# Performance work log

Measured on AMD Instinct MI355X. Metric: run time of the kernel, lower is better.

Reference implementation:

```python
import jax, jax.numpy as jnp
import numpy as np

D_MODEL = 512
NUM_HEADS = 8
WINDOW = 64
HEAD_DIM = D_MODEL // NUM_HEADS


def setup_inputs() -> dict:
    key = jax.random.key(0)
    k1, k2, k3 = jax.random.split(key, 3)
    B, F, L, D = 4, 16, 2048, D_MODEL
    x = jax.random.normal(k1, (B, F, L, D), dtype=jnp.float32)
    w_qkv = jax.random.normal(k2, (D, 3 * D), dtype=jnp.float32) * (1.0 / np.sqrt(D))
    b_qkv = jnp.zeros((3 * D,), dtype=jnp.float32)
    w_proj = jax.random.normal(k3, (D, D), dtype=jnp.float32) * (1.0 / np.sqrt(D))
    b_proj = jnp.zeros((D,), dtype=jnp.float32)
    return {"x": x, "w_qkv": w_qkv, "b_qkv": b_qkv, "w_proj": w_proj, "b_proj": b_proj}


def reference(x, w_qkv, b_qkv, w_proj, b_proj):
    B, F, L, D = x.shape
    W = WINDOW
    H, hd = NUM_HEADS, HEAD_DIM
    nw = L // W  # L chosen divisible by window_size; pad path is identity here
    # partition into windows: (B, F, nw, W, D)
    xw = x.reshape(B, F, nw, W, D)
    # fused QKV projection
    qkv = jnp.einsum('bfnwd,de->bfnwe', xw, w_qkv) + b_qkv  # (B,F,nw,W,3D)
    qkv = qkv.reshape(B, F, nw, W, 3, H, hd)
    q = qkv[..., 0, :, :]  # (B,F,nw,W,H,hd)
    k = qkv[..., 1, :, :]
    v = qkv[..., 2, :, :]
    scale = 1.0 / np.sqrt(hd).astype(np.float32)
    # per-window attention: scores (B,F,nw,H,W,W)
    scores = jnp.einsum('bfnqhd,bfnkhd->bfnhqk', q, k) * scale
    attn = jax.nn.softmax(scores, axis=-1)
    out = jnp.einsum('bfnhqk,bfnkhd->bfnqhd', attn, v)  # (B,F,nw,W,H,hd)
    out = out.reshape(B, F, nw, W, D)
    out = jnp.einsum('bfnwd,de->bfnwe', out, w_proj) + b_proj
    return out.reshape(B, F, L, D)
```

## Files before the change

### kernel.cpp

```cpp
#include <hip/hip_runtime.h>

typedef __attribute__((ext_vector_type(8))) short short8;
typedef __attribute__((ext_vector_type(4))) float f32x4;
typedef unsigned short u16;
typedef unsigned int u32;

__device__ __forceinline__ u16 f2bf(float f){
  union { float f; u32 u; } v; v.f = f;
  u32 u = v.u;
  u32 r = (u + 0x7FFFu + ((u >> 16) & 1u)) >> 16;
  return (u16)r;
}

__device__ __forceinline__ int swz(int row, int cb){ return cb ^ ((row & 7) << 4); }

__device__ __forceinline__ void gload16(const void* g, void* l){
  __builtin_amdgcn_global_load_lds(
      (const __attribute__((address_space(1))) unsigned int*)g,
      (__attribute__((address_space(3))) unsigned int*)l, 16, 0, 0);
}

__global__ void convert_weights_swz(const float* __restrict__ wqkv,
                                    const float* __restrict__ wproj,
                                    u16* __restrict__ wq_swz,
                                    u16* __restrict__ wpt){
  int c = blockIdx.x * 256 + threadIdx.x;
  union { u16 u[8]; uint4 v; } t;
  if (c < 98304){
    int tile = c >> 10, row = (c >> 3) & 127, c7 = c & 7;
    int bn = tile >> 3, kt = tile & 7;
    int j  = c7 ^ (row & 7);
    int e  = bn * 128 + row;
    int k0 = kt * 64 + j * 8;
    #pragma unroll
    for (int i = 0; i < 8; ++i) t.u[i] = f2bf(wqkv[(long)(k0 + i) * 1536 + e]);
    *reinterpret_cast<uint4*>(wq_swz + (long)c * 8) = t.v;
  } else {
    int t2 = c - 98304;
    int cc = t2 >> 6;
    int kc = (t2 & 63) << 3;
    #pragma unroll
    for (int i = 0; i < 8; ++i) t.u[i] = f2bf(wproj[(long)(kc + i) * 512 + cc]);
    *reinterpret_cast<uint4*>(wpt + (long)cc * 512 + kc) = t.v;
  }
}

__global__ void convert_x(const float* __restrict__ x, u16* __restrict__ xbf){
  int c = blockIdx.x * 256 + threadIdx.x;
  int tile = c >> 10, row = (c >> 3) & 127, c7 = c & 7;
  int bm = tile >> 3, kt = tile & 7;
  int j  = c7 ^ (row & 7);
  const float* src = x + (long)(bm * 128 + row) * 512 + kt * 64 + j * 8;
  float4 v0 = *reinterpret_cast<const float4*>(src);
  float4 v1 = *reinterpret_cast<const float4*>(src + 4);
  union { u16 u[8]; uint4 v; } t;
  t.u[0] = f2bf(v0.x); t.u[1] = f2bf(v0.y); t.u[2] = f2bf(v0.z); t.u[3] = f2bf(v0.w);
  t.u[4] = f2bf(v1.x); t.u[5] = f2bf(v1.y); t.u[6] = f2bf(v1.z); t.u[7] = f2bf(v1.w);
  *reinterpret_cast<uint4*>(xbf + (long)c * 8) = t.v;
}

__global__ __launch_bounds__(256) void qkv_gemm(
    const u16*  __restrict__ xbf,
    const u16*  __restrict__ wswz,
    const float* __restrict__ bqkv,
    u16* __restrict__ qkv)
{
  __shared__ char smem[34816];
  char* ldsA = smem;
  char* ldsB = smem + 16384;
  u16*  ldsC = (u16*)smem;

  int hb   = blockIdx.x;
  int work = (hb & 7) * 1536 + (hb >> 3);
  int bn   = work % 12;
  int bm   = work / 12;

  const int tid = threadIdx.x;
  const int l = tid & 63, w = tid >> 6;
  const int g = l >> 4,  ln = l & 15;
  const int wm = w >> 1, wn = w & 1;

  f32x4 acc[4][4];
  #pragma unroll
  for (int m = 0; m < 4; ++m)
    #pragma unroll
    for (int n = 0; n < 4; ++n) acc[m][n] = (f32x4){0.f,0.f,0.f,0.f};

  const char* abase = (const char*)(xbf  + (long)(bm * 8) * 8192);
  const char* bbase = (const char*)(wswz + (long)(bn * 8) * 8192);

  for (int kt = 0; kt < 8; ++kt){
    __syncthreads();
    #pragma unroll
    for (int i = 0; i < 4; ++i){
      gload16(abase + (long)kt*16384 + (i*256 + tid)*16, ldsA + (i*256 + w*64)*16);
      gload16(bbase + (long)kt*16384 + (i*256 + tid)*16, ldsB + (i*256 + w*64)*16);
    }
    __syncthreads();
    #pragma unroll
    for (int ks = 0; ks < 2; ++ks){
      short8 a[4], b[4];
      #pragma unroll
      for (int m = 0; m < 4; ++m){
        int row = wm*64 + m*16 + ln;
        a[m] = *reinterpret_cast<const short8*>(ldsA + row*128 + (((ks*4 + g) ^ (row & 7)) << 4));
      }
      #pragma unroll
      for (int n = 0; n < 4; ++n){
        int row = wn*64 + n*16 + ln;
        b[n] = *reinterpret_cast<const short8*>(ldsB + row*128 + (((ks*4 + g) ^ (row & 7)) << 4));
      }
      #pragma unroll
      for (int m = 0; m < 4; ++m)
        #pragma unroll
        for (int n = 0; n < 4; ++n)
          acc[m][n] = __builtin_amdgcn_mfma_f32_16x16x32_bf16(a[m], b[n], acc[m][n], 0, 0, 0);
    }
  }

  __syncthreads();
  #pragma unroll
  for (int n = 0; n < 4; ++n){
    int col  = wn*64 + n*16 + ln;
    float bias = bqkv[bn*128 + col];
    #pragma unroll
    for (int m = 0; m < 4; ++m){
      int r0 = wm*64 + m*16 + g*4;
      #pragma unroll
      for (int r = 0; r < 4; ++r)
        ldsC[(r0 + r) * 136 + col] = f2bf(acc[m][n][r] + bias);
    }
  }
  __syncthreads();
  {
    int row = tid >> 1, half = tid & 1;
    const char* src = (const char*)(ldsC + row * 136 + half * 64);
    char* dst = (char*)qkv + ((long)(bm*128 + row) * 1536 + bn*128 + half*64) * 2;
    #pragma unroll
    for (int j = 0; j < 8; ++j)
      *reinterpret_cast<uint4*>(dst + j*16) = *reinterpret_cast<const uint4*>(src + j*16);
  }
}

__global__ __launch_bounds__(512, 2) void winattn_proj(
    const u16* __restrict__ qkv,
    const u16* __restrict__ wpt,
    const float* __restrict__ bproj,
    float* __restrict__ out)
{
  __shared__ u16 lds[8][2][4096];
  const int tid = threadIdx.x;
  const int l = tid & 63, w = tid >> 6;
  const int g = l >> 4,  ln = l & 15;
  const long tokb = (long)blockIdx.x * 64;
  u16* vt = lds[w][0];
  u16* pp = lds[w][1];
  const int h = w;

  short8 qa[4][2], kb[4][2];
  #pragma unroll
  for (int m = 0; m < 4; ++m){
    const char* qrow = (const char*)(qkv + (tokb + m*16 + ln) * 1536 + h*64 + g*8);
    const char* krow = (const char*)(qkv + (tokb + m*16 + ln) * 1536 + 512 + h*64 + g*8);
    qa[m][0] = *reinterpret_cast<const short8*>(qrow);
    qa[m][1] = *reinterpret_cast<const short8*>(qrow + 64);
    kb[m][0] = *reinterpret_cast<const short8*>(krow);
    kb[m][1] = *reinterpret_cast<const short8*>(krow + 64);
  }
  const int dg = l & 3, tg = l >> 2;
  uint4 vr[4][2];
  #pragma unroll
  for (int r = 0; r < 4; ++r){
    const char* vrow = (const char*)(qkv + (tokb + tg*4 + r) * 1536 + 1024 + h*64 + dg*16);
    vr[r][0] = *reinterpret_cast<const uint4*>(vrow);
    vr[r][1] = *reinterpret_cast<const uint4*>(vrow + 16);
  }
  f32x4 sacc[4][4];
  #pragma unroll
  for (int m = 0; m < 4; ++m)
    #pragma unroll
    for (int n = 0; n < 4; ++n) sacc[m][n] = (f32x4){0.f,0.f,0.f,0.f};
  #pragma unroll
  for (int ks = 0; ks < 2; ++ks)
    #pragma unroll
    for (int m = 0; m < 4; ++m)
      #pragma unroll
      for (int n = 0; n < 4; ++n)
        sacc[m][n] = __builtin_amdgcn_mfma_f32_16x16x32_bf16(qa[m][ks], kb[n][ks], sacc[m][n], 0, 0, 0);
  #pragma unroll
  for (int dd = 0; dd < 16; ++dd){
    int d = dg*16 + dd;
    int sub = dd & 7, hh = dd >> 3;
    uint2 pk;
    pk.x = (u32)((const u16*)&vr[0][hh])[sub] | ((u32)((const u16*)&vr[1][hh])[sub] << 16);
    pk.y = (u32)((const u16*)&vr[2][hh])[sub] | ((u32)((const u16*)&vr[3][hh])[sub] << 16);
    *reinterpret_cast<uint2*>((char*)vt + d*128 + swz(d, tg*8)) = pk;
  }
  #pragma unroll
  for (int m = 0; m < 4; ++m){
    #pragma unroll
    for (int r = 0; r < 4; ++r){
      float mx = fmaxf(fmaxf(sacc[m][0][r], sacc[m][1][r]), fmaxf(sacc[m][2][r], sacc[m][3][r]));
      mx = fmaxf(mx, __shfl_xor(mx, 1, 64));
      mx = fmaxf(mx, __shfl_xor(mx, 2, 64));
      mx = fmaxf(mx, __shfl_xor(mx, 4, 64));
      mx = fmaxf(mx, __shfl_xor(mx, 8, 64));
      float p[4], s = 0.f;
      #pragma unroll
      for (int n = 0; n < 4; ++n){
        p[n] = __expf((sacc[m][n][r] - mx) * 0.125f);
        s += p[n];
      }
      s += __shfl_xor(s, 1, 64);
      s += __shfl_xor(s, 2, 64);
      s += __shfl_xor(s, 4, 64);
      s += __shfl_xor(s, 8, 64);
      float inv = 1.f / s;
      int i = m*16 + g*4 + r;
      #pragma unroll
      for (int n = 0; n < 4; ++n){
        int c = n*16 + ln;
        *reinterpret_cast<u16*>((char*)pp + i*128 + swz(i, c*2)) = f2bf(p[n] * inv);
      }
    }
  }
  f32x4 oacc[4][4];
  #pragma unroll
  for (int m = 0; m < 4; ++m)
    #pragma unroll
    for (int n = 0; n < 4; ++n) oacc[m][n] = (f32x4){0.f,0.f,0.f,0.f};
  #pragma unroll
  for (int ks = 0; ks < 2; ++ks){
    short8 pa[4], vb[4];
    #pragma unroll
    for (int m = 0; m < 4; ++m){
      int row = m*16 + ln;
      pa[m] = *reinterpret_cast<const short8*>((char*)pp + row*128 + swz(row, (ks*32 + g*8)*2));
    }
    #pragma unroll
    for (int n = 0; n < 4; ++n){
      int row = n*16 + ln;
      vb[n] = *reinterpret_cast<const short8*>((char*)vt + row*128 + swz(row, (ks*32 + g*8)*2));
    }
    #pragma unroll
    for (int m = 0; m < 4; ++m)
      #pragma unroll
      for (int n = 0; n < 4; ++n)
        oacc[m][n] = __builtin_amdgcn_mfma_f32_16x16x32_bf16(pa[m], vb[n], oacc[m][n], 0, 0, 0);
  }
  #pragma unroll
  for (int m = 0; m < 4; ++m)
    #pragma unroll
    for (int n = 0; n < 4; ++n){
      int d = n*16 + ln;
      #pragma unroll
      for (int r = 0; r < 4; ++r){
        int t = m*16 + g*4 + r;
        *reinterpret_cast<u16*>((char*)pp + t*128 + swz(t, d*2)) = f2bf(oacc[m][n][r]);
      }
    }

  __syncthreads();

  f32x4 acc[4][4];
  #pragma unroll
  for (int m = 0; m < 4; ++m)
    #pragma unroll
    for (int n = 0; n < 4; ++n) acc[m][n] = (f32x4){0.f,0.f,0.f,0.f};

  for (int hh = 0; hh < 8; ++hh){
    const char* obuf = (const char*)lds[hh][1];
    #pragma unroll
    for (int ks = 0; ks < 2; ++ks){
      short8 a[4], b[4];
      #pragma unroll
      for (int m = 0; m < 4; ++m){
        int row = m*16 + ln;
        a[m] = *reinterpret_cast<const short8*>(obuf + row*128 + swz(row, (ks*32 + g*8)*2));
      }
      #pragma unroll
      for (int n = 0; n < 4; ++n){
        int e = w*64 + n*16 + ln;
        b[n] = *reinterpret_cast<const short8*>(wpt + (long)e*512 + hh*64 + ks*32 + g*8);
      }
      #pragma unroll
      for (int m = 0; m < 4; ++m)
        #pragma unroll
        for (int n = 0; n < 4; ++n)
          acc[m][n] = __builtin_amdgcn_mfma_f32_16x16x32_bf16(a[m], b[n], acc[m][n], 0, 0, 0);
    }
  }

  #pragma unroll
  for (int n = 0; n < 4; ++n){
    int col = w*64 + n*16 + ln;
    float bias = bproj[col];
    #pragma unroll
    for (int m = 0; m < 4; ++m){
      #pragma unroll
      for (int r = 0; r < 4; ++r){
        int t = m*16 + g*4 + r;
        out[(tokb + t) * 512 + col] = acc[m][n][r] + bias;
      }
    }
  }
}

__global__ void convert_weights(const float* __restrict__ wqkv,
                                const float* __restrict__ wproj,
                                u16* __restrict__ wqkvt,
                                u16* __restrict__ wprojt){
  int tid = blockIdx.x * 256 + threadIdx.x;
  union { u16 u[8]; uint4 v; } tmp;
  if (tid < 1536 * 64){
    int e  = tid >> 6;
    int kc = (tid & 63) << 3;
    #pragma unroll
    for (int i = 0; i < 8; ++i) tmp.u[i] = f2bf(wqkv[(long)(kc + i) * 1536 + e]);
    *reinterpret_cast<uint4*>(wqkvt + (long)e * 512 + kc) = tmp.v;
  } else {
    int t2 = tid - 1536 * 64;
    int c  = t2 >> 6;
    int kc = (t2 & 63) << 3;
    #pragma unroll
    for (int i = 0; i < 8; ++i) tmp.u[i] = f2bf(wproj[(long)(kc + i) * 512 + c]);
    *reinterpret_cast<uint4*>(wprojt + (long)c * 512 + kc) = tmp.v;
  }
}

__global__ __launch_bounds__(512, 2) void fused_winattn(
    const float* __restrict__ x,
    const u16*  __restrict__ wqkvt,
    const float* __restrict__ bqkv,
    const u16*  __restrict__ wprojt,
    const float* __restrict__ bproj,
    float* __restrict__ out)
{
  __shared__ u16 lds_x[64 * 512];
  __shared__ u16 lds_q[64 * 64];
  __shared__ u16 lds_k[64 * 64];
  __shared__ u16 lds_vt[64 * 64];
  __shared__ u16 lds_p[64 * 64];

  const int tid = threadIdx.x;
  const int l   = tid & 63;
  const int w   = tid >> 6;
  const int g   = l >> 4;
  const int ln  = l & 15;
  const long tokbase = (long)blockIdx.x * 64;

  {
    const float4* xv = reinterpret_cast<const float4*>(x + tokbase * 512);
    #pragma unroll
    for (int j = 0; j < 16; ++j){
      int i   = j * 512 + tid;
      int row = i >> 7;
      int c4  = i & 127;
      float4 v = xv[i];
      uint2 pk;
      pk.x = (u32)f2bf(v.x) | ((u32)f2bf(v.y) << 16);
      pk.y = (u32)f2bf(v.z) | ((u32)f2bf(v.w) << 16);
      int byte = row * 1024 + swz(row, c4 * 8);
      *reinterpret_cast<uint2*>(reinterpret_cast<char*>(lds_x) + byte) = pk;
    }
  }

  f32x4 oacc[4][4];
  #pragma unroll
  for (int m = 0; m < 4; ++m)
    #pragma unroll
    for (int n = 0; n < 4; ++n) oacc[m][n] = (f32x4){0.f, 0.f, 0.f, 0.f};

  const int mw   = w & 3;
  const int half = w >> 2;

  __syncthreads();

  for (int h = 0; h < 8; ++h){
    f32x4 qacc[6];
    #pragma unroll
    for (int j = 0; j < 6; ++j) qacc[j] = (f32x4){0.f, 0.f, 0.f, 0.f};
    int ebase[6];
    #pragma unroll
    for (int j = 0; j < 6; ++j){
      int nt = half * 6 + j;
      int sec = nt >> 2;
      ebase[j] = sec * 512 + h * 64 + (nt & 3) * 16;
    }
    const int arow = mw * 16 + ln;
    #pragma unroll
    for (int ks = 0; ks < 16; ++ks){
      short8 a = *reinterpret_cast<const short8*>(
          reinterpret_cast<const char*>(lds_x) + arow * 1024 + swz(arow, (ks * 32 + g * 8) * 2));
      #pragma unroll
      for (int j = 0; j < 6; ++j){
        short8 b = *reinterpret_cast<const short8*>(
            wqkvt + (long)(ebase[j] + ln) * 512 + ks * 32 + g * 8);
        qacc[j] = __builtin_amdgcn_mfma_f32_16x16x32_bf16(a, b, qacc[j], 0, 0, 0);
      }
    }
    #pragma unroll
    for (int j = 0; j < 6; ++j){
      int nt  = half * 6 + j;
      int sec = nt >> 2;
      float bias = bqkv[ebase[j] + ln];
      if (sec < 2){
        u16* dst = (sec == 0) ? lds_q : lds_k;
        int c = (nt & 3) * 16 + ln;
        #pragma unroll
        for (int r = 0; r < 4; ++r){
          int t = mw * 16 + g * 4 + r;
          int byte = t * 128 + swz(t, c * 2);
          *reinterpret_cast<u16*>(reinterpret_cast<char*>(dst) + byte) = f2bf(qacc[j][r] + bias);
        }
      } else {
        int d  = (nt & 3) * 16 + ln;
        int t0 = mw * 16 + g * 4;
        uint2 pk;
        pk.x = (u32)f2bf(qacc[j][0] + bias) | ((u32)f2bf(qacc[j][1] + bias) << 16);
        pk.y = (u32)f2bf(qacc[j][2] + bias) | ((u32)f2bf(qacc[j][3] + bias) << 16);
        int byte = d * 128 + swz(d, t0 * 2);
        *reinterpret_cast<uint2*>(reinterpret_cast<char*>(lds_vt) + byte) = pk;
      }
    }
    __syncthreads();

    if (w < 4){
      f32x4 sacc[4];
      #pragma unroll
      for (int jt = 0; jt < 4; ++jt) sacc[jt] = (f32x4){0.f, 0.f, 0.f, 0.f};
      #pragma unroll
      for (int ks = 0; ks < 2; ++ks){
        int qrow = w * 16 + ln;
        short8 a = *reinterpret_cast<const short8*>(
            reinterpret_cast<const char*>(lds_q) + qrow * 128 + swz(qrow, (ks * 32 + g * 8) * 2));
        #pragma unroll
        for (int jt = 0; jt < 4; ++jt){
          int krow = jt * 16 + ln;
          short8 b = *reinterpret_cast<const short8*>(
              reinterpret_cast<const char*>(lds_k) + krow * 128 + swz(krow, (ks * 32 + g * 8) * 2));
          sacc[jt] = __builtin_amdgcn_mfma_f32_16x16x32_bf16(a, b, sacc[jt], 0, 0, 0);
        }
      }
      #pragma unroll
      for (int r = 0; r < 4; ++r){
        float mx = fmaxf(fmaxf(sacc[0][r], sacc[1][r]), fmaxf(sacc[2][r], sacc[3][r]));
        mx = fmaxf(mx, __shfl_xor(mx, 1, 64));
        mx = fmaxf(mx, __shfl_xor(mx, 2, 64));
        mx = fmaxf(mx, __shfl_xor(mx, 4, 64));
        mx = fmaxf(mx, __shfl_xor(mx, 8, 64));
        float p[4], s = 0.f;
        #pragma unroll
        for (int jt = 0; jt < 4; ++jt){
          p[jt] = __expf((sacc[jt][r] - mx) * 0.125f);
          s += p[jt];
        }
        s += __shfl_xor(s, 1, 64);
        s += __shfl_xor(s, 2, 64);
        s += __shfl_xor(s, 4, 64);
        s += __shfl_xor(s, 8, 64);
        float inv = 1.f / s;
        int i = w * 16 + g * 4 + r;
        #pragma unroll
        for (int jt = 0; jt < 4; ++jt){
          int c = jt * 16 + ln;
          int byte = i * 128 + swz(i, c * 2);
          *reinterpret_cast<u16*>(reinterpret_cast<char*>(lds_p) + byte) = f2bf(p[jt] * inv);
        }
      }
    }
    __syncthreads();

    {
      int mc  = w & 3;
      int nc0 = (w >> 2) * 2;
      f32x4 oc[2];
      oc[0] = (f32x4){0.f, 0.f, 0.f, 0.f};
      oc[1] = (f32x4){0.f, 0.f, 0.f, 0.f};
      #pragma unroll
      for (int ks = 0; ks < 2; ++ks){
        int prow = mc * 16 + ln;
        short8 a = *reinterpret_cast<const short8*>(
            reinterpret_cast<const char*>(lds_p) + prow * 128 + swz(prow, (ks * 32 + g * 8) * 2));
        #pragma unroll
        for (int jj = 0; jj < 2; ++jj){
          int vrow = (nc0 + jj) * 16 + ln;
          short8 b = *reinterpret_cast<const short8*>(
              reinterpret_cast<const char*>(lds_vt) + vrow * 128 + swz(vrow, (ks * 32 + g * 8) * 2));
          oc[jj] = __builtin_amdgcn_mfma_f32_16x16x32_bf16(a, b, oc[jj], 0, 0, 0);
        }
      }
      #pragma unroll
      for (int jj = 0; jj < 2; ++jj){
        int d = (nc0 + jj) * 16 + ln;
        #pragma unroll
        for (int r = 0; r < 4; ++r){
          int t = mc * 16 + g * 4 + r;
          int byte = t * 128 + swz(t, d * 2);
          *reinterpret_cast<u16*>(reinterpret_cast<char*>(lds_q) + byte) = f2bf(oc[jj][r]);
        }
      }
    }
    __syncthreads();

    #pragma unroll
    for (int ks = 0; ks < 2; ++ks){
      short8 a[4];
      #pragma unroll
      for (int m = 0; m < 4; ++m){
        int row = m * 16 + ln;
        a[m] = *reinterpret_cast<const short8*>(
            reinterpret_cast<const char*>(lds_q) + row * 128 + swz(row, (ks * 32 + g * 8) * 2));
      }
      #pragma unroll
      for (int nt = 0; nt < 4; ++nt){
        int e = w * 64 + nt * 16 + ln;
        short8 b = *reinterpret_cast<const short8*>(
            wprojt + (long)e * 512 + h * 64 + ks * 32 + g * 8);
        #pragma unroll
        for (int m = 0; m < 4; ++m)
          oacc[m][nt] = __builtin_amdgcn_mfma_f32_16x16x32_bf16(a[m], b, oacc[m][nt], 0, 0, 0);
      }
    }
    __syncthreads();
  }

  #pragma unroll
  for (int nt = 0; nt < 4; ++nt){
    int col = w * 64 + nt * 16 + ln;
    float bias = bproj[col];
    #pragma unroll
    for (int m = 0; m < 4; ++m){
      #pragma unroll
      for (int r = 0; r < 4; ++r){
        int t = m * 16 + g * 4 + r;
        out[(tokbase + t) * 512 + col] = oacc[m][nt][r] + bias;
      }
    }
  }
}

extern "C" void kernel_launch(void* const* d_in, const int* in_sizes, int n_in,
                              void* d_out, int out_size, void* d_ws, size_t ws_size,
                              hipStream_t stream) {
  const float* x     = (const float*)d_in[0];
  const float* wqkv  = (const float*)d_in[1];
  const float* bqkv  = (const float*)d_in[2];
  const float* wproj = (const float*)d_in[3];
  const float* bproj = (const float*)d_in[4];
  float* out = (float*)d_out;

  const size_t NEED = 538968064ULL;
  if (ws_size >= NEED){
    u16* wq_swz = (u16*)d_ws;
    u16* wpt    = (u16*)((char*)d_ws + 1572864);
    u16* xbf    = (u16*)((char*)d_ws + 2097152);
    u16* qkv    = (u16*)((char*)d_ws + 136314880);
    convert_weights_swz<<<512, 256, 0, stream>>>(wqkv, wproj, wq_swz, wpt);
    convert_x<<<32768, 256, 0, stream>>>(x, xbf);
    qkv_gemm<<<12288, 256, 0, stream>>>(xbf, wq_swz, bqkv, qkv);
    winattn_proj<<<2048, 512, 0, stream>>>(qkv, wpt, bproj, out);
  } else {
    u16* wqkvt  = (u16*)d_ws;
    u16* wprojt = wqkvt + 1536 * 512;
    convert_weights<<<512, 256, 0, stream>>>(wqkv, wproj, wqkvt, wprojt);
    fused_winattn<<<2048, 512, 0, stream>>>(x, wqkvt, bqkv, wprojt, bproj, out);
  }
}
```

Before: 686.2 us.

## Keep softmax probabilities in registers via transposed scores and lane shuffles

Scores are now computed as K·Qᵀ, so each query's softmax reduction runs over only two cross-lane shuffles. The normalized probabilities are packed to bf16 with v_cvt_pk_bf16_f32 and rearranged into MFMA A-operand layout with shuffles, instead of round-tripping through a per-wave LDS buffer. This halves shared memory per block, and the launch bound is raised to 4 blocks per CU. s_setprio is placed around the MFMA loops. The tighter register budget implied by the higher launch bound risks spills.

New measurement: 662.6 us. -3.4%, faster.

```diff
diff --git a/kernel.cpp b/kernel.cpp
--- a/kernel.cpp
+++ b/kernel.cpp
@@ -10,6 +10,12 @@
   u32 u = v.u;
   u32 r = (u + 0x7FFFu + ((u >> 16) & 1u)) >> 16;
   return (u16)r;
+}
+
+__device__ __forceinline__ u32 cvtpk(float a, float b){
+  u32 r;
+  asm("v_cvt_pk_bf16_f32 %0, %1, %2" : "=v"(r) : "v"(a), "v"(b));
+  return r;
 }
 
 __device__ __forceinline__ int swz(int row, int cb){ return cb ^ ((row & 7) << 4); }
@@ -142,112 +148,137 @@
   }
 }
 
-__global__ __launch_bounds__(512, 2) void winattn_proj(
+__global__ __launch_bounds__(512, 4) void winattn_proj(
     const u16* __restrict__ qkv,
     const u16* __restrict__ wpt,
     const float* __restrict__ bproj,
     float* __restrict__ out)
 {
-  __shared__ u16 lds[8][2][4096];
+  __shared__ u16 lds[8][4096];
   const int tid = threadIdx.x;
   const int l = tid & 63, w = tid >> 6;
   const int g = l >> 4,  ln = l & 15;
+  const int gh = g >> 1, gl = g & 1;
   const long tokb = (long)blockIdx.x * 64;
-  u16* vt = lds[w][0];
-  u16* pp = lds[w][1];
+  u16* vt = lds[w];
   const int h = w;
 
-  short8 qa[4][2], kb[4][2];
-  #pragma unroll
-  for (int m = 0; m < 4; ++m){
-    const char* qrow = (const char*)(qkv + (tokb + m*16 + ln) * 1536 + h*64 + g*8);
-    const char* krow = (const char*)(qkv + (tokb + m*16 + ln) * 1536 + 512 + h*64 + g*8);
-    qa[m][0] = *reinterpret_cast<const short8*>(qrow);
-    qa[m][1] = *reinterpret_cast<const short8*>(qrow + 64);
-    kb[m][0] = *reinterpret_cast<const short8*>(krow);
-    kb[m][1] = *reinterpret_cast<const short8*>(krow + 64);
-  }
-  const int dg = l & 3, tg = l >> 2;
-  uint4 vr[4][2];
-  #pragma unroll
-  for (int r = 0; r < 4; ++r){
-    const char* vrow = (const char*)(qkv + (tokb + tg*4 + r) * 1536 + 1024 + h*64 + dg*16);
-    vr[r][0] = *reinterpret_cast<const uint4*>(vrow);
-    vr[r][1] = *reinterpret_cast<const uint4*>(vrow + 16);
-  }
-  f32x4 sacc[4][4];
+  {
+    const int dg = l & 3, tg = l >> 2;
+    uint4 vr[4][2];
+    #pragma unroll
+    for (int r = 0; r < 4; ++r){
+      const char* vrow = (const char*)(qkv + (tokb + tg*4 + r) * 1536 + 1024 + h*64 + dg*16);
+      vr[r][0] = *reinterpret_cast<const uint4*>(vrow);
+      vr[r][1] = *reinterpret_cast<const uint4*>(vrow + 16);
+    }
+    #pragma unroll
+    for (int dd = 0; dd < 16; ++dd){
+      int d = dg*16 + dd;
+      int sub = dd & 7, hi = dd >> 3;
+      uint2 pk;
+      pk.x = (u32)((const u16*)&vr[0][hi])[sub] | ((u32)((const u16*)&vr[1][hi])[sub] << 16);
+      pk.y = (u32)((const u16*)&vr[2][hi])[sub] | ((u32)((const u16*)&vr[3][hi])[sub] << 16);
+      *reinterpret_cast<uint2*>((char*)vt + d*128 + swz(d, tg*8)) = pk;
+    }
+  }
+
+  f32x4 oacc[4][4];
   #pragma unroll
   for (int m = 0; m < 4; ++m)
     #pragma unroll
-    for (int n = 0; n < 4; ++n) sacc[m][n] = (f32x4){0.f,0.f,0.f,0.f};
-  #pragma unroll
-  for (int ks = 0; ks < 2; ++ks)
-    #pragma unroll
-    for (int m = 0; m < 4; ++m)
-      #pragma unroll
-      for (int n = 0; n < 4; ++n)
-        sacc[m][n] = __builtin_amdgcn_mfma_f32_16x16x32_bf16(qa[m][ks], kb[n][ks], sacc[m][n], 0, 0, 0);
-  #pragma unroll
-  for (int dd = 0; dd < 16; ++dd){
-    int d = dg*16 + dd;
-    int sub = dd & 7, hh = dd >> 3;
-    uint2 pk;
-    pk.x = (u32)((const u16*)&vr[0][hh])[sub] | ((u32)((const u16*)&vr[1][hh])[sub] << 16);
-    pk.y = (u32)((const u16*)&vr[2][hh])[sub] | ((u32)((const u16*)&vr[3][hh])[sub] << 16);
-    *reinterpret_cast<uint2*>((char*)vt + d*128 + swz(d, tg*8)) = pk;
-  }
-  #pragma unroll
-  for (int m = 0; m < 4; ++m){
-    #pragma unroll
-    for (int r = 0; r < 4; ++r){
-      float mx = fmaxf(fmaxf(sacc[m][0][r], sacc[m][1][r]), fmaxf(sacc[m][2][r], sacc[m][3][r]));
-      mx = fmaxf(mx, __shfl_xor(mx, 1, 64));
-      mx = fmaxf(mx, __shfl_xor(mx, 2, 64));
-      mx = fmaxf(mx, __shfl_xor(mx, 4, 64));
-      mx = fmaxf(mx, __shfl_xor(mx, 8, 64));
-      float p[4], s = 0.f;
+    for (int n = 0; n < 4; ++n) oacc[m][n] = (f32x4){0.f,0.f,0.f,0.f};
+
+  const int lnA = ln + 32*gl;
+
+  #pragma unroll
+  for (int half = 0; half < 2; ++half){
+    short8 qa[2][2];
+    #pragma unroll
+    for (int j = 0; j < 2; ++j){
+      const char* qrow = (const char*)(qkv + (tokb + (half*2+j)*16 + ln) * 1536 + h*64 + g*8);
+      qa[j][0] = *reinterpret_cast<const short8*>(qrow);
+      qa[j][1] = *reinterpret_cast<const short8*>(qrow + 64);
+    }
+    f32x4 st[4][2];
+    #pragma unroll
+    for (int mk = 0; mk < 4; ++mk){
+      st[mk][0] = (f32x4){0.f,0.f,0.f,0.f};
+      st[mk][1] = (f32x4){0.f,0.f,0.f,0.f};
+    }
+    #pragma unroll
+    for (int mk = 0; mk < 4; ++mk){
+      const char* krow = (const char*)(qkv + (tokb + mk*16 + ln) * 1536 + 512 + h*64 + g*8);
+      short8 kb0 = *reinterpret_cast<const short8*>(krow);
+      short8 kb1 = *reinterpret_cast<const short8*>(krow + 64);
+      #pragma unroll
+      for (int j = 0; j < 2; ++j){
+        st[mk][j] = __builtin_amdgcn_mfma_f32_16x16x32_bf16(kb0, qa[j][0], st[mk][j], 0, 0, 0);
+        st[mk][j] = __builtin_amdgcn_mfma_f32_16x16x32_bf16(kb1, qa[j][1], st[mk][j], 0, 0, 0);
+      }
+    }
+    u32 warr[4][2][2];
+    #pragma unroll
+    for (int j = 0; j < 2; ++j){
+      float mx = -3.4e38f;
+      #pragma unroll
+      for (int mk = 0; mk < 4; ++mk)
+        #pragma unroll
+        for (int r = 0; r < 4; ++r) mx = fmaxf(mx, st[mk][j][r]);
+      mx = fmaxf(mx, __shfl_xor(mx, 16, 64));
+      mx = fmaxf(mx, __shfl_xor(mx, 32, 64));
+      float s = 0.f;
+      #pragma unroll
+      for (int mk = 0; mk < 4; ++mk)
+        #pragma unroll
+        for (int r = 0; r < 4; ++r){
+          float p = __expf((st[mk][j][r] - mx) * 0.125f);
+          st[mk][j][r] = p; s += p;
+        }
+      s += __shfl_xor(s, 16, 64);
+      s += __shfl_xor(s, 32, 64);
+      float inv = 1.f / s;
+      #pragma unroll
+      for (int mk = 0; mk < 4; ++mk){
+        warr[mk][j][0] = cvtpk(st[mk][j][0]*inv, st[mk][j][1]*inv);
+        warr[mk][j][1] = cvtpk(st[mk][j][2]*inv, st[mk][j][3]*inv);
+      }
+    }
+    __builtin_amdgcn_s_setprio(1);
+    #pragma unroll
+    for (int ks = 0; ks < 2; ++ks){
+      short8 vb[4];
       #pragma unroll
       for (int n = 0; n < 4; ++n){
-        p[n] = __expf((sacc[m][n][r] - mx) * 0.125f);
-        s += p[n];
-      }
-      s += __shfl_xor(s, 1, 64);
-      s += __shfl_xor(s, 2, 64);
-      s += __shfl_xor(s, 4, 64);
-      s += __shfl_xor(s, 8, 64);
-      float inv = 1.f / s;
-      int i = m*16 + g*4 + r;
-      #pragma unroll
-      for (int n = 0; n < 4; ++n){
-        int c = n*16 + ln;
-        *reinterpret_cast<u16*>((char*)pp + i*128 + swz(i, c*2)) = f2bf(p[n] * inv);
-      }
-    }
-  }
-  f32x4 oacc[4][4];
-  #pragma unroll
-  for (int m = 0; m < 4; ++m)
-    #pragma unroll
-    for (int n = 0; n < 4; ++n) oacc[m][n] = (f32x4){0.f,0.f,0.f,0.f};
-  #pragma unroll
-  for (int ks = 0; ks < 2; ++ks){
-    short8 pa[4], vb[4];
-    #pragma unroll
-    for (int m = 0; m < 4; ++m){
-      int row = m*16 + ln;
-      pa[m] = *reinterpret_cast<const short8*>((char*)pp + row*128 + swz(row, (ks*32 + g*8)*2));
-    }
-    #pragma unroll
-    for (int n = 0; n < 4; ++n){
-      int row = n*16 + ln;
-      vb[n] = *reinterpret_cast<const short8*>((char*)vt + row*128 + swz(row, (ks*32 + g*8)*2));
-    }
-    #pragma unroll
-    for (int m = 0; m < 4; ++m)
-      #pragma unroll
-      for (int n = 0; n < 4; ++n)
-        oacc[m][n] = __builtin_amdgcn_mfma_f32_16x16x32_bf16(pa[m], vb[n], oacc[m][n], 0, 0, 0);
-  }
+        int row = n*16 + ln;
+        vb[n] = *reinterpret_cast<const short8*>((char*)vt + row*128 + swz(row, (ks*32 + g*8)*2));
+      }
+      #pragma unroll
+      for (int mo = 0; mo < 2; ++mo){
+        int m = half*2 + mo;
+        u32 c0a = warr[2*ks  ][mo][0], c0b = warr[2*ks  ][mo][1];
+        u32 c1a = warr[2*ks+1][mo][0], c1b = warr[2*ks+1][mo][1];
+        u32 s0a = (u32)__shfl((int)c0a, lnA, 64);
+        u32 s1a = (u32)__shfl((int)c1a, lnA, 64);
+        u32 s0b = (u32)__shfl((int)c0b, lnA, 64);
+        u32 s1b = (u32)__shfl((int)c1b, lnA, 64);
+        u32 t0a = (u32)__shfl((int)c0a, lnA+16, 64);
+        u32 t1a = (u32)__shfl((int)c1a, lnA+16, 64);
+        u32 t0b = (u32)__shfl((int)c0b, lnA+16, 64);
+        u32 t1b = (u32)__shfl((int)c1b, lnA+16, 64);
+        union { u32 u[4]; short8 v; } pf;
+        pf.u[0] = gh ? s1a : s0a;
+        pf.u[1] = gh ? s1b : s0b;
+        pf.u[2] = gh ? t1a : t0a;
+        pf.u[3] = gh ? t1b : t0b;
+        #pragma unroll
+        for (int n = 0; n < 4; ++n)
+          oacc[m][n] = __builtin_amdgcn_mfma_f32_16x16x32_bf16(pf.v, vb[n], oacc[m][n], 0, 0, 0);
+      }
+    }
+    __builtin_amdgcn_s_setprio(0);
+  }
+
   #pragma unroll
   for (int m = 0; m < 4; ++m)
     #pragma unroll
@@ -256,7 +287,7 @@
       #pragma unroll
       for (int r = 0; r < 4; ++r){
         int t = m*16 + g*4 + r;
-        *reinterpret_cast<u16*>((char*)pp + t*128 + swz(t, d*2)) = f2bf(oacc[m][n][r]);
+        *reinterpret_cast<u16*>((char*)vt + t*128 + swz(t, d*2)) = f2bf(oacc[m][n][r]);
       }
     }
 
@@ -269,7 +300,7 @@
     for (int n = 0; n < 4; ++n) acc[m][n] = (f32x4){0.f,0.f,0.f,0.f};
 
   for (int hh = 0; hh < 8; ++hh){
-    const char* obuf = (const char*)lds[hh][1];
+    const char* obuf = (const char*)lds[hh];
     #pragma unroll
     for (int ks = 0; ks < 2; ++ks){
       short8 a[4], b[4];
@@ -283,11 +314,13 @@
         int e = w*64 + n*16 + ln;
         b[n] = *reinterpret_cast<const short8*>(wpt + (long)e*512 + hh*64 + ks*32 + g*8);
       }
+      __builtin_amdgcn_s_setprio(1);
       #pragma unroll
       for (int m = 0; m < 4; ++m)
         #pragma unroll
         for (int n = 0; n < 4; ++n)
           acc[m][n] = __builtin_amdgcn_mfma_f32_16x16x32_bf16(a[m], b[n], acc[m][n], 0, 0, 0);
+      __builtin_amdgcn_s_setprio(0);
     }
   }
 
```
